# Kernel optimization log

Measured on AMD Instinct MI355X. Metric: run time of the kernel, lower is better.

## Reference

```python
import jax, jax.numpy as jnp
import numpy as np

N_NODES = 100000
N_EDGES = 1200000
NFEAT = 64
NHID = 64
NCLASS = 16
BN_EPS = 1e-5
L2_EPS = 1e-12


def setup_inputs() -> dict:
    key = jax.random.key(0)
    ks = jax.random.split(key, 8)
    edge_index = jax.random.randint(ks[0], (2, N_EDGES), 0, N_NODES, dtype=jnp.int64)
    x = jax.random.normal(ks[1], (N_NODES, NFEAT), dtype=jnp.float32)
    # SAGEConv params: lin_l (neighbor path, has bias), lin_r (root path, no bias)
    W_l = jax.random.normal(ks[2], (NHID, NFEAT), dtype=jnp.float32) * (1.0 / np.sqrt(NFEAT))
    b_l = jnp.zeros((NHID,), dtype=jnp.float32)
    W_r = jax.random.normal(ks[3], (NHID, NFEAT), dtype=jnp.float32) * (1.0 / np.sqrt(NFEAT))
    # BatchNorm1d affine params
    gamma = jnp.ones((NHID,), dtype=jnp.float32)
    beta = jnp.zeros((NHID,), dtype=jnp.float32)
    # final fc (xavier-ish scale, zero bias per weights_init)
    W_fc = jax.random.normal(ks[4], (NCLASS, NHID), dtype=jnp.float32) * (1.0 / np.sqrt(NHID))
    b_fc = jnp.zeros((NCLASS,), dtype=jnp.float32)
    return {"edge_index": edge_index, "x": x, "W_l": W_l, "b_l": b_l,
            "W_r": W_r, "gamma": gamma, "beta": beta, "W_fc": W_fc, "b_fc": b_fc}


def reference(edge_index, x, W_l, b_l, W_r, gamma, beta, W_fc, b_fc):
    N = x.shape[0]
    src, dst = edge_index[0], edge_index[1]
    # SAGEConv mean aggregation: gather x at source nodes, scatter-mean to dst
    msgs = x[src]                                                  # [E, F]
    sums = jax.ops.segment_sum(msgs, dst, num_segments=N)         # [N, F]
    cnt = jax.ops.segment_sum(jnp.ones((src.shape[0], 1), x.dtype), dst, num_segments=N)
    mean = sums / jnp.maximum(cnt, 1.0)
    # out = lin_l(mean_neighbors) + lin_r(x_root)
    h = mean @ W_l.T + b_l + x @ W_r.T                              # [N, H]
    # normalize=True -> L2 normalize rows (F.normalize semantics)
    h = h / jnp.maximum(jnp.linalg.norm(h, axis=-1, keepdims=True), L2_EPS)
    # transition: ReLU -> BatchNorm1d (training stats) -> Dropout (identity in eval)
    h = jax.nn.relu(h)
    mu = jnp.mean(h, axis=0)
    var = jnp.var(h, axis=0)
    h = (h - mu) / jnp.sqrt(var + BN_EPS) * gamma + beta
    return h @ W_fc.T + b_fc                                        # [N, C]
```

## Files before the change

kernel.cpp:

```cpp
#include <hip/hip_runtime.h>
#include <hip/hip_bf16.h>


typedef __attribute__((ext_vector_type(8))) short short8;
typedef __attribute__((ext_vector_type(4))) float f32x4;

__device__ __forceinline__ unsigned short f2bf(float f) {
    unsigned int u = __builtin_bit_cast(unsigned int, f);
    u += 0x7FFFu + ((u >> 16) & 1u);
    return (unsigned short)(u >> 16);
}
__device__ __forceinline__ float bf2f(unsigned short s) {
    return __builtin_bit_cast(float, ((unsigned int)s) << 16);
}

#define CHUNK 8192

__device__ __forceinline__ int exclScan256(int v, int* swv) {
    const int t = threadIdx.x, lane = t & 63, wid = t >> 6;
    __syncthreads();
    int s = v;
#pragma unroll
    for (int off = 1; off < 64; off <<= 1) {
        int tt = __shfl_up(s, off);
        if (lane >= off) s += tt;
    }
    if (lane == 63) swv[wid] = s;
    __syncthreads();
    if (t == 0) {
        int a = 0;
#pragma unroll
        for (int w = 0; w < 4; ++w) { int tt = swv[w]; swv[w] = a; a += tt; }
    }
    __syncthreads();
    return s - v + swv[wid];
}

__global__ __launch_bounds__(256) void k_prep(const int* __restrict__ eidx,
                                              int* __restrict__ cnt,
                                              const float4* __restrict__ x4,
                                              ushort4* __restrict__ xbf,
                                              int E, int NB, int NBLK,
                                              int n4, int do_x) {
    __shared__ int lh[256];
    const int tid = threadIdx.x;
    if ((int)blockIdx.x < NBLK) {
        lh[tid] = 0;
        __syncthreads();
        const int base = blockIdx.x * CHUNK;
        for (int i = tid; i < CHUNK; i += 256) {
            int e = base + i;
            if (e < E) atomicAdd(&lh[eidx[E + e] >> 9], 1);
        }
        __syncthreads();
        if (tid < NB) cnt[(size_t)tid * NBLK + blockIdx.x] = lh[tid];
    } else if (do_x) {
        int t = ((int)blockIdx.x - NBLK) * 256 + tid;
        if (t < n4) {
            float4 v = x4[t];
            xbf[t] = make_ushort4(f2bf(v.x), f2bf(v.y), f2bf(v.z), f2bf(v.w));
        }
    }
}

__global__ __launch_bounds__(256) void k_scanbkt(int* __restrict__ cnt,
                                                 int* __restrict__ btot,
                                                 int NBLK) {
    __shared__ int swv[4];
    const int b = blockIdx.x;
    const int t = threadIdx.x;
    int v = (t < NBLK) ? cnt[(size_t)b * NBLK + t] : 0;
    int excl = exclScan256(v, swv);
    if (t < NBLK) cnt[(size_t)b * NBLK + t] = excl;
    if (t == 255) btot[b] = excl + v;
}

__global__ __launch_bounds__(256) void k_bscatter(const int* __restrict__ eidx,
                                                  const int* __restrict__ cnt,
                                                  const int* __restrict__ btot,
                                                  unsigned int* __restrict__ ebuf,
                                                  int E, int NB, int NBLK) {
    __shared__ int cur[256];
    __shared__ int swv[4];
    const int tid = threadIdx.x;
    int bv = (tid < NB) ? btot[tid] : 0;
    int bexcl = exclScan256(bv, swv);
    if (tid < NB)
        cur[tid] = bexcl + cnt[(size_t)tid * NBLK + blockIdx.x];
    __syncthreads();
    const int base = blockIdx.x * CHUNK;
    for (int i = tid; i < CHUNK; i += 256) {
        int e = base + i;
        if (e < E) {
            int d = eidx[E + e];
            int s = eidx[e];
            int p = atomicAdd(&cur[d >> 9], 1);
            ebuf[p] = (unsigned int)s | ((unsigned int)(d & 511) << 17);
        }
    }
}

__global__ __launch_bounds__(256) void k_bfinal(const unsigned int* __restrict__ ebuf,
                                                const int* __restrict__ btot,
                                                int* __restrict__ rowptr,
                                                int* __restrict__ colv,
                                                int N, int NB, int E) {
    __shared__ int h[512];
    __shared__ int swv[4];
    __shared__ int sseg[2];
    const int b = blockIdx.x;
    const int tid = threadIdx.x;
    int bv = (tid < NB) ? btot[tid] : 0;
    int bexcl = exclScan256(bv, swv);
    if (tid == b) { sseg[0] = bexcl; sseg[1] = bexcl + bv; }
    h[2 * tid] = 0;
    h[2 * tid + 1] = 0;
    __syncthreads();
    const int segb = sseg[0], sege = sseg[1];
    for (int i = segb + tid; i < sege; i += 256)
        atomicAdd(&h[ebuf[i] >> 17], 1);
    __syncthreads();
    int a0 = h[2 * tid], a1 = h[2 * tid + 1];
    int ts = a0 + a1;
    const int lane = tid & 63, wid = tid >> 6;
    int s = ts;
#pragma unroll
    for (int off = 1; off < 64; off <<= 1) {
        int tt = __shfl_up(s, off);
        if (lane >= off) s += tt;
    }
    if (lane == 63) swv[wid] = s;
    __syncthreads();
    if (tid == 0) {
        int a = 0;
#pragma unroll
        for (int w = 0; w < 4; ++w) { int tt = swv[w]; swv[w] = a; a += tt; }
    }
    __syncthreads();
    int excl = s - ts + swv[wid];
    h[2 * tid] = excl;
    h[2 * tid + 1] = excl + a0;
    int node = b * 512 + 2 * tid;
    if (node < N) rowptr[node] = segb + excl;
    if (node + 1 < N) rowptr[node + 1] = segb + excl + a0;
    __syncthreads();
    for (int i = segb + tid; i < sege; i += 256) {
        unsigned int u = ebuf[i];
        int p = atomicAdd(&h[u >> 17], 1);
        colv[segb + p] = (int)(u & 0x1FFFFu);
    }
    if (b == 0 && tid == 0) rowptr[N] = E;
}

__device__ __forceinline__ void acc8(float a[8], uint4 v) {
    a[0] += bf2f((unsigned short)(v.x & 0xFFFFu));
    a[1] += bf2f((unsigned short)(v.x >> 16));
    a[2] += bf2f((unsigned short)(v.y & 0xFFFFu));
    a[3] += bf2f((unsigned short)(v.y >> 16));
    a[4] += bf2f((unsigned short)(v.z & 0xFFFFu));
    a[5] += bf2f((unsigned short)(v.z >> 16));
    a[6] += bf2f((unsigned short)(v.w & 0xFFFFu));
    a[7] += bf2f((unsigned short)(v.w >> 16));
}

__global__ __launch_bounds__(256) void k_gfused(
        const unsigned short* __restrict__ xbf,
        const int* __restrict__ rowptr, const int* __restrict__ colv,
        const float* __restrict__ Wl, const float* __restrict__ bl,
        const float* __restrict__ Wr,
        unsigned short* __restrict__ mh,
        float* __restrict__ pstats, int N) {
    __shared__ float sRed[4][128];

    const int tid = threadIdx.x;
    const int wid = tid >> 6;
    const int lane = tid & 63;
    const int l15 = lane & 15;
    const int quad = lane >> 4;

    const int tbase = blockIdx.x * 64 + wid * 16;
    const int mrow = tbase + l15;
    const int mld = (mrow < N) ? mrow : (N - 1);

    const int gb = rowptr[mld], ge = rowptr[mld + 1];
    float g0[8], g1[8];
#pragma unroll
    for (int j = 0; j < 8; ++j) { g0[j] = 0.f; g1[j] = 0.f; }
    const unsigned short* xrow = xbf + quad * 8;
    int p = gb;
    for (; p + 2 <= ge; p += 2) {
        int s0 = colv[p], s1 = colv[p + 1];
        uint4 v00 = *(const uint4*)(xrow + (size_t)s0 * 64);
        uint4 v01 = *(const uint4*)(xrow + (size_t)s0 * 64 + 32);
        uint4 v10 = *(const uint4*)(xrow + (size_t)s1 * 64);
        uint4 v11 = *(const uint4*)(xrow + (size_t)s1 * 64 + 32);
        acc8(g0, v00); acc8(g1, v01);
        acc8(g0, v10); acc8(g1, v11);
    }
    for (; p < ge; ++p) {
        int s0 = colv[p];
        uint4 v00 = *(const uint4*)(xrow + (size_t)s0 * 64);
        uint4 v01 = *(const uint4*)(xrow + (size_t)s0 * 64 + 32);
        acc8(g0, v00); acc8(g1, v01);
    }
    const float inv = 1.0f / fmaxf((float)(ge - gb), 1.0f);
    short8 afr[2];
    {
        union { short8 v; unsigned short u[8]; } pk;
#pragma unroll
        for (int j = 0; j < 8; ++j) pk.u[j] = f2bf(g0[j] * inv);
        afr[0] = pk.v;
#pragma unroll
        for (int j = 0; j < 8; ++j) pk.u[j] = f2bf(g1[j] * inv);
        afr[1] = pk.v;
    }

    short8 rfr[2];
    rfr[0] = *(const short8*)(xbf + (size_t)mld * 64 + quad * 8);
    rfr[1] = *(const short8*)(xbf + (size_t)mld * 64 + 32 + quad * 8);

    short8 bfrag[4][4];
#pragma unroll
    for (int c = 0; c < 4; ++c) {
#pragma unroll
        for (int f = 0; f < 4; ++f) {
            const int n = f * 16 + l15;
            const float* wsrc = (c < 2)
                ? (Wl + (size_t)n * 64 + c * 32 + quad * 8)
                : (Wr + (size_t)n * 64 + (c - 2) * 32 + quad * 8);
            float4 w0 = *(const float4*)wsrc;
            float4 w1 = *(const float4*)(wsrc + 4);
            union { short8 v; unsigned short u[8]; } pk;
            pk.u[0] = f2bf(w0.x); pk.u[1] = f2bf(w0.y);
            pk.u[2] = f2bf(w0.z); pk.u[3] = f2bf(w0.w);
            pk.u[4] = f2bf(w1.x); pk.u[5] = f2bf(w1.y);
            pk.u[6] = f2bf(w1.z); pk.u[7] = f2bf(w1.w);
            bfrag[c][f] = pk.v;
        }
    }
    float blv[4];
#pragma unroll
    for (int f = 0; f < 4; ++f) blv[f] = bl[f * 16 + l15];

    f32x4 acc[4] = {{0.f, 0.f, 0.f, 0.f}, {0.f, 0.f, 0.f, 0.f},
                    {0.f, 0.f, 0.f, 0.f}, {0.f, 0.f, 0.f, 0.f}};
#pragma unroll
    for (int c = 0; c < 2; ++c)
#pragma unroll
        for (int f = 0; f < 4; ++f)
            acc[f] = __builtin_amdgcn_mfma_f32_16x16x32_bf16(afr[c], bfrag[c][f], acc[f], 0, 0, 0);
#pragma unroll
    for (int c = 0; c < 2; ++c)
#pragma unroll
        for (int f = 0; f < 4; ++f)
            acc[f] = __builtin_amdgcn_mfma_f32_16x16x32_bf16(rfr[c], bfrag[c + 2][f], acc[f], 0, 0, 0);

    float psum[4] = {0.f, 0.f, 0.f, 0.f};
    float psq[4] = {0.f, 0.f, 0.f, 0.f};
#pragma unroll
    for (int reg = 0; reg < 4; ++reg) {
        const int node = tbase + quad * 4 + reg;
        float hv[4];
        float ss = 0.f;
#pragma unroll
        for (int f = 0; f < 4; ++f) {
            hv[f] = acc[f][reg] + blv[f];
            ss += hv[f] * hv[f];
        }
        ss += __shfl_xor(ss, 1);
        ss += __shfl_xor(ss, 2);
        ss += __shfl_xor(ss, 4);
        ss += __shfl_xor(ss, 8);
        float sc = 1.0f / fmaxf(sqrtf(ss), 1e-12f);
        if (node < N) {
#pragma unroll
            for (int f = 0; f < 4; ++f) {
                float r = fmaxf(hv[f] * sc, 0.f);
                unsigned short rb = f2bf(r);
                float e = bf2f(rb);
                mh[(size_t)node * 64 + f * 16 + l15] = rb;
                psum[f] += e;
                psq[f] += e * e;
            }
        }
    }

#pragma unroll
    for (int f = 0; f < 4; ++f) {
        psum[f] += __shfl_xor(psum[f], 16);
        psum[f] += __shfl_xor(psum[f], 32);
        psq[f] += __shfl_xor(psq[f], 16);
        psq[f] += __shfl_xor(psq[f], 32);
    }
    if (lane < 16) {
#pragma unroll
        for (int f = 0; f < 4; ++f) {
            sRed[wid][f * 16 + l15] = psum[f];
            sRed[wid][64 + f * 16 + l15] = psq[f];
        }
    }
    __syncthreads();
    if (tid < 128) {
        float v = sRed[0][tid] + sRed[1][tid] + sRed[2][tid] + sRed[3][tid];
        pstats[(size_t)blockIdx.x * 128 + tid] = v;
    }
}

__global__ __launch_bounds__(256) void k_gather_f32(
        const float4* __restrict__ x4, const int* __restrict__ rowptr,
        const int* __restrict__ colv, ushort4* __restrict__ mh, int N) {
    int t = blockIdx.x * 256 + threadIdx.x;
    int n = t >> 4;
    int l = t & 15;
    if (n >= N) return;
    int b = rowptr[n], e = rowptr[n + 1];
    float ax = 0.f, ay = 0.f, az = 0.f, aw = 0.f;
    int p = b;
    for (; p + 4 <= e; p += 4) {
        int s0 = colv[p], s1 = colv[p + 1], s2 = colv[p + 2], s3 = colv[p + 3];
        float4 v0 = x4[(size_t)s0 * 16 + l];
        float4 v1 = x4[(size_t)s1 * 16 + l];
        float4 v2 = x4[(size_t)s2 * 16 + l];
        float4 v3 = x4[(size_t)s3 * 16 + l];
        ax += (v0.x + v1.x) + (v2.x + v3.x);
        ay += (v0.y + v1.y) + (v2.y + v3.y);
        az += (v0.z + v1.z) + (v2.z + v3.z);
        aw += (v0.w + v1.w) + (v2.w + v3.w);
    }
    for (; p < e; ++p) {
        int s0 = colv[p];
        float4 v0 = x4[(size_t)s0 * 16 + l];
        ax += v0.x; ay += v0.y; az += v0.z; aw += v0.w;
    }
    float inv = 1.0f / fmaxf((float)(e - b), 1.0f);
    mh[(size_t)n * 16 + l] = make_ushort4(f2bf(ax * inv), f2bf(ay * inv),
                                          f2bf(az * inv), f2bf(aw * inv));
}

__global__ __launch_bounds__(256) void k_fused_legacy(
        const float* __restrict__ x,
        const float* __restrict__ Wl, const float* __restrict__ bl,
        const float* __restrict__ Wr,
        unsigned short* __restrict__ mh,
        float* __restrict__ pstats, int N) {
    __shared__ float sRed[4][128];
    const int tid = threadIdx.x;
    const int wid = tid >> 6;
    const int lane = tid & 63;
    const int l15 = lane & 15;
    const int quad = lane >> 4;

    short8 bfrag[4][4];
#pragma unroll
    for (int c = 0; c < 4; ++c) {
#pragma unroll
        for (int f = 0; f < 4; ++f) {
            const int n = f * 16 + l15;
            const float* wsrc = (c < 2)
                ? (Wl + (size_t)n * 64 + c * 32 + quad * 8)
                : (Wr + (size_t)n * 64 + (c - 2) * 32 + quad * 8);
            float4 w0 = *(const float4*)wsrc;
            float4 w1 = *(const float4*)(wsrc + 4);
            union { short8 v; unsigned short u[8]; } pk;
            pk.u[0] = f2bf(w0.x); pk.u[1] = f2bf(w0.y);
            pk.u[2] = f2bf(w0.z); pk.u[3] = f2bf(w0.w);
            pk.u[4] = f2bf(w1.x); pk.u[5] = f2bf(w1.y);
            pk.u[6] = f2bf(w1.z); pk.u[7] = f2bf(w1.w);
            bfrag[c][f] = pk.v;
        }
    }
    float blv[4];
#pragma unroll
    for (int f = 0; f < 4; ++f) blv[f] = bl[f * 16 + l15];

    const int tbase = blockIdx.x * 64 + wid * 16;
    const int mrow = tbase + l15;
    const int mld = (mrow < N) ? mrow : (N - 1);
    f32x4 acc[4] = {{0.f, 0.f, 0.f, 0.f}, {0.f, 0.f, 0.f, 0.f},
                    {0.f, 0.f, 0.f, 0.f}, {0.f, 0.f, 0.f, 0.f}};
#pragma unroll
    for (int c = 0; c < 2; ++c) {
        short8 a = *(const short8*)(mh + (size_t)mld * 64 + c * 32 + quad * 8);
#pragma unroll
        for (int f = 0; f < 4; ++f)
            acc[f] = __builtin_amdgcn_mfma_f32_16x16x32_bf16(a, bfrag[c][f], acc[f], 0, 0, 0);
    }
#pragma unroll
    for (int c = 0; c < 2; ++c) {
        const float* xp = x + (size_t)mld * 64 + c * 32 + quad * 8;
        float4 a0 = *(const float4*)xp;
        float4 a1 = *(const float4*)(xp + 4);
        union { short8 v; unsigned short u[8]; } pk;
        pk.u[0] = f2bf(a0.x); pk.u[1] = f2bf(a0.y);
        pk.u[2] = f2bf(a0.z); pk.u[3] = f2bf(a0.w);
        pk.u[4] = f2bf(a1.x); pk.u[5] = f2bf(a1.y);
        pk.u[6] = f2bf(a1.z); pk.u[7] = f2bf(a1.w);
#pragma unroll
        for (int f = 0; f < 4; ++f)
            acc[f] = __builtin_amdgcn_mfma_f32_16x16x32_bf16(pk.v, bfrag[c + 2][f], acc[f], 0, 0, 0);
    }

    float psum[4] = {0.f, 0.f, 0.f, 0.f};
    float psq[4] = {0.f, 0.f, 0.f, 0.f};
#pragma unroll
    for (int reg = 0; reg < 4; ++reg) {
        const int node = tbase + quad * 4 + reg;
        float hv[4];
        float ss = 0.f;
#pragma unroll
        for (int f = 0; f < 4; ++f) {
            hv[f] = acc[f][reg] + blv[f];
            ss += hv[f] * hv[f];
        }
        ss += __shfl_xor(ss, 1);
        ss += __shfl_xor(ss, 2);
        ss += __shfl_xor(ss, 4);
        ss += __shfl_xor(ss, 8);
        float sc = 1.0f / fmaxf(sqrtf(ss), 1e-12f);
        if (node < N) {
#pragma unroll
            for (int f = 0; f < 4; ++f) {
                float r = fmaxf(hv[f] * sc, 0.f);
                unsigned short rb = f2bf(r);
                float e = bf2f(rb);
                mh[(size_t)node * 64 + f * 16 + l15] = rb;
                psum[f] += e;
                psq[f] += e * e;
            }
        }
    }
#pragma unroll
    for (int f = 0; f < 4; ++f) {
        psum[f] += __shfl_xor(psum[f], 16);
        psum[f] += __shfl_xor(psum[f], 32);
        psq[f] += __shfl_xor(psq[f], 16);
        psq[f] += __shfl_xor(psq[f], 32);
    }
    if (lane < 16) {
#pragma unroll
        for (int f = 0; f < 4; ++f) {
            sRed[wid][f * 16 + l15] = psum[f];
            sRed[wid][64 + f * 16 + l15] = psq[f];
        }
    }
    __syncthreads();
    if (tid < 128) {
        float v = sRed[0][tid] + sRed[1][tid] + sRed[2][tid] + sRed[3][tid];
        pstats[(size_t)blockIdx.x * 128 + tid] = v;
    }
}

__global__ __launch_bounds__(64) void k_stats(const float* __restrict__ pstats,
                                              float* __restrict__ stats, int nblk) {
    int col = blockIdx.x;
    int l = threadIdx.x;
    float s = 0.f;
    for (int r = l; r < nblk; r += 64) s += pstats[(size_t)r * 128 + col];
    s += __shfl_xor(s, 1);
    s += __shfl_xor(s, 2);
    s += __shfl_xor(s, 4);
    s += __shfl_xor(s, 8);
    s += __shfl_xor(s, 16);
    s += __shfl_xor(s, 32);
    if (l == 0) stats[col] = s;
}

__global__ __launch_bounds__(256) void k_out(
        const unsigned short* __restrict__ h, const float* __restrict__ stats,
        const float* __restrict__ gamma, const float* __restrict__ beta,
        const float* __restrict__ Wfc, const float* __restrict__ bfc,
        float* __restrict__ out, int N) {
    __shared__ float sWm[64 * 16];
    __shared__ float sShift[64];
    __shared__ float sBase[16];
    const int tid = threadIdx.x;
    const float invN = 1.0f / (float)N;
    if (tid < 64) {
        float mu = stats[tid] * invN;
        float var = stats[64 + tid] * invN - mu * mu;
        float sc = gamma[tid] / sqrtf(var + 1e-5f);
        sShift[tid] = beta[tid] - mu * sc;
#pragma unroll
        for (int c = 0; c < 16; ++c) sWm[tid * 16 + c] = Wfc[c * 64 + tid] * sc;
    }
    __syncthreads();
    if (tid < 16) {
        float b = bfc[tid];
#pragma unroll
        for (int j = 0; j < 64; ++j) b += sShift[j] * Wfc[tid * 64 + j];
        sBase[tid] = b;
    }
    __syncthreads();
    int g = blockIdx.x * 256 + tid;
    int n = g >> 4;
    int c = g & 15;
    if (n >= N) return;
    const ushort4* h4 = (const ushort4*)(h + (size_t)n * 64);
    float acc = sBase[c];
#pragma unroll
    for (int jq = 0; jq < 16; ++jq) {
        ushort4 v = h4[jq];
        acc += bf2f(v.x) * sWm[(jq * 4 + 0) * 16 + c];
        acc += bf2f(v.y) * sWm[(jq * 4 + 1) * 16 + c];
        acc += bf2f(v.z) * sWm[(jq * 4 + 2) * 16 + c];
        acc += bf2f(v.w) * sWm[(jq * 4 + 3) * 16 + c];
    }
    out[(size_t)n * 16 + c] = acc;
}

extern "C" void kernel_launch(void* const* d_in, const int* in_sizes, int n_in,
                              void* d_out, int out_size, void* d_ws, size_t ws_size,
                              hipStream_t stream) {
    const int* eidx = (const int*)d_in[0];
    const float* x = (const float*)d_in[1];
    const float* Wl = (const float*)d_in[2];
    const float* bl = (const float*)d_in[3];
    const float* Wr = (const float*)d_in[4];
    const float* gamma = (const float*)d_in[5];
    const float* beta = (const float*)d_in[6];
    const float* Wfc = (const float*)d_in[7];
    const float* bfc = (const float*)d_in[8];
    float* out = (float*)d_out;

    const int E = in_sizes[0] / 2;
    const int N = in_sizes[1] / 64;
    const int NB = (N + 511) >> 9;
    const int NBLK = (E + CHUNK - 1) / CHUNK;
    const int fb = (N + 63) / 64;
    const int n4 = N * 16;

    int* cnt = (int*)d_ws;
    int* btot = cnt + (size_t)NB * NBLK;
    int* rowptr = btot + NB;
    float* pstats = (float*)(rowptr + N + 1);
    float* stats = pstats + (size_t)fb * 128;
    int* colv = (int*)(stats + 128);
    unsigned int* ebuf = (unsigned int*)(colv + E);
    unsigned short* mh = (unsigned short*)(((uintptr_t)(ebuf + E) + 15) & ~(uintptr_t)15);
    unsigned short* xbf = mh + (size_t)N * 64;

    size_t need_bf = (size_t)((char*)(xbf + (size_t)N * 64) - (char*)d_ws);
    const int use_bf = (ws_size >= need_bf) ? 1 : 0;

    int cbl = use_bf ? (n4 + 255) / 256 : 0;
    k_prep<<<NBLK + cbl, 256, 0, stream>>>(eidx, cnt, (const float4*)x,
                                           (ushort4*)xbf, E, NB, NBLK, n4, use_bf);
    k_scanbkt<<<NB, 256, 0, stream>>>(cnt, btot, NBLK);
    k_bscatter<<<NBLK, 256, 0, stream>>>(eidx, cnt, btot, ebuf, E, NB, NBLK);
    k_bfinal<<<NB, 256, 0, stream>>>(ebuf, btot, rowptr, colv, N, NB, E);

    if (use_bf) {
        k_gfused<<<fb, 256, 0, stream>>>(xbf, rowptr, colv, Wl, bl, Wr,
                                         mh, pstats, N);
    } else {
        int gblocks = (int)(((size_t)N * 16 + 255) / 256);
        k_gather_f32<<<gblocks, 256, 0, stream>>>((const float4*)x, rowptr, colv,
                                                  (ushort4*)mh, N);
        k_fused_legacy<<<fb, 256, 0, stream>>>(x, Wl, bl, Wr, mh, pstats, N);
    }

    k_stats<<<128, 64, 0, stream>>>(pstats, stats, fb);

    int oblocks = (int)(((size_t)N * 16 + 255) / 256);
    k_out<<<oblocks, 256, 0, stream>>>(mh, stats, gamma, beta, Wfc, bfc, out, N);
}
```

Before: 231.0 us.

## Spread neighbor gather across 16 lanes per node and stage means in LDS

The fused gather+GEMM kernel now processes 16 nodes per block. All 256 threads gather neighbor rows, with 16 lanes per node each loading 8 bytes, instead of one lane per node loading 128 bytes. The bf16 means go through shared memory, and a single wave then runs the MFMA projection with the weight fragments converted inline. This raises memory-level parallelism in the irregular gather, but leaves three of four waves idle during the MFMA and normalization phase. It also multiplies the number of blocks, weight loads and partial-stat rows that k_stats must reduce.

```diff
diff --git a/kernel.cpp b/kernel.cpp
--- a/kernel.cpp
+++ b/kernel.cpp
@@ -152,17 +152,6 @@
     if (b == 0 && tid == 0) rowptr[N] = E;
 }
 
-__device__ __forceinline__ void acc8(float a[8], uint4 v) {
-    a[0] += bf2f((unsigned short)(v.x & 0xFFFFu));
-    a[1] += bf2f((unsigned short)(v.x >> 16));
-    a[2] += bf2f((unsigned short)(v.y & 0xFFFFu));
-    a[3] += bf2f((unsigned short)(v.y >> 16));
-    a[4] += bf2f((unsigned short)(v.z & 0xFFFFu));
-    a[5] += bf2f((unsigned short)(v.z >> 16));
-    a[6] += bf2f((unsigned short)(v.w & 0xFFFFu));
-    a[7] += bf2f((unsigned short)(v.w >> 16));
-}
-
 __global__ __launch_bounds__(256) void k_gfused(
         const unsigned short* __restrict__ xbf,
         const int* __restrict__ rowptr, const int* __restrict__ colv,
@@ -170,56 +159,68 @@
         const float* __restrict__ Wr,
         unsigned short* __restrict__ mh,
         float* __restrict__ pstats, int N) {
-    __shared__ float sRed[4][128];
+    __shared__ unsigned short sm[16][72];
 
     const int tid = threadIdx.x;
-    const int wid = tid >> 6;
-    const int lane = tid & 63;
+    const int tbase = blockIdx.x * 16;
+
+    {
+        const int nloc = tid >> 4;
+        const int l = tid & 15;
+        const int mrow = tbase + nloc;
+        const int mld = (mrow < N) ? mrow : (N - 1);
+        const uint2* xbf2 = (const uint2*)xbf;
+        int b = rowptr[mld], e = rowptr[mld + 1];
+        float a0 = 0.f, a1 = 0.f, a2 = 0.f, a3 = 0.f;
+        int p = b;
+        for (; p + 4 <= e; p += 4) {
+            int s0 = colv[p], s1 = colv[p + 1], s2 = colv[p + 2], s3 = colv[p + 3];
+            uint2 v0 = xbf2[(size_t)s0 * 16 + l];
+            uint2 v1 = xbf2[(size_t)s1 * 16 + l];
+            uint2 v2 = xbf2[(size_t)s2 * 16 + l];
+            uint2 v3 = xbf2[(size_t)s3 * 16 + l];
+            a0 += bf2f((unsigned short)(v0.x & 0xFFFF)) + bf2f((unsigned short)(v1.x & 0xFFFF)) +
+                  bf2f((unsigned short)(v2.x & 0xFFFF)) + bf2f((unsigned short)(v3.x & 0xFFFF));
+            a1 += bf2f((unsigned short)(v0.x >> 16)) + bf2f((unsigned short)(v1.x >> 16)) +
+                  bf2f((unsigned short)(v2.x >> 16)) + bf2f((unsigned short)(v3.x >> 16));
+            a2 += bf2f((unsigned short)(v0.y & 0xFFFF)) + bf2f((unsigned short)(v1.y & 0xFFFF)) +
+                  bf2f((unsigned short)(v2.y & 0xFFFF)) + bf2f((unsigned short)(v3.y & 0xFFFF));
+            a3 += bf2f((unsigned short)(v0.y >> 16)) + bf2f((unsigned short)(v1.y >> 16)) +
+                  bf2f((unsigned short)(v2.y >> 16)) + bf2f((unsigned short)(v3.y >> 16));
+        }
+        for (; p < e; ++p) {
+            int s0 = colv[p];
+            uint2 v0 = xbf2[(size_t)s0 * 16 + l];
+            a0 += bf2f((unsigned short)(v0.x & 0xFFFF));
+            a1 += bf2f((unsigned short)(v0.x >> 16));
+            a2 += bf2f((unsigned short)(v0.y & 0xFFFF));
+            a3 += bf2f((unsigned short)(v0.y >> 16));
+        }
+        float inv = 1.0f / fmaxf((float)(e - b), 1.0f);
+        *(ushort4*)&sm[nloc][l * 4] = make_ushort4(f2bf(a0 * inv), f2bf(a1 * inv),
+                                                   f2bf(a2 * inv), f2bf(a3 * inv));
+    }
+    __syncthreads();
+    if (tid >= 64) return;
+
+    const int lane = tid;
     const int l15 = lane & 15;
     const int quad = lane >> 4;
 
-    const int tbase = blockIdx.x * 64 + wid * 16;
-    const int mrow = tbase + l15;
-    const int mld = (mrow < N) ? mrow : (N - 1);
-
-    const int gb = rowptr[mld], ge = rowptr[mld + 1];
-    float g0[8], g1[8];
-#pragma unroll
-    for (int j = 0; j < 8; ++j) { g0[j] = 0.f; g1[j] = 0.f; }
-    const unsigned short* xrow = xbf + quad * 8;
-    int p = gb;
-    for (; p + 2 <= ge; p += 2) {
-        int s0 = colv[p], s1 = colv[p + 1];
-        uint4 v00 = *(const uint4*)(xrow + (size_t)s0 * 64);
-        uint4 v01 = *(const uint4*)(xrow + (size_t)s0 * 64 + 32);
-        uint4 v10 = *(const uint4*)(xrow + (size_t)s1 * 64);
-        uint4 v11 = *(const uint4*)(xrow + (size_t)s1 * 64 + 32);
-        acc8(g0, v00); acc8(g1, v01);
-        acc8(g0, v10); acc8(g1, v11);
-    }
-    for (; p < ge; ++p) {
-        int s0 = colv[p];
-        uint4 v00 = *(const uint4*)(xrow + (size_t)s0 * 64);
-        uint4 v01 = *(const uint4*)(xrow + (size_t)s0 * 64 + 32);
-        acc8(g0, v00); acc8(g1, v01);
-    }
-    const float inv = 1.0f / fmaxf((float)(ge - gb), 1.0f);
-    short8 afr[2];
-    {
-        union { short8 v; unsigned short u[8]; } pk;
-#pragma unroll
-        for (int j = 0; j < 8; ++j) pk.u[j] = f2bf(g0[j] * inv);
-        afr[0] = pk.v;
-#pragma unroll
-        for (int j = 0; j < 8; ++j) pk.u[j] = f2bf(g1[j] * inv);
-        afr[1] = pk.v;
-    }
-
-    short8 rfr[2];
-    rfr[0] = *(const short8*)(xbf + (size_t)mld * 64 + quad * 8);
-    rfr[1] = *(const short8*)(xbf + (size_t)mld * 64 + 32 + quad * 8);
-
-    short8 bfrag[4][4];
+    short8 afr[2], rfr[2];
+    afr[0] = *(const short8*)&sm[l15][quad * 8];
+    afr[1] = *(const short8*)&sm[l15][32 + quad * 8];
+    const int rrow = tbase + l15;
+    const int rld = (rrow < N) ? rrow : (N - 1);
+    rfr[0] = *(const short8*)(xbf + (size_t)rld * 64 + quad * 8);
+    rfr[1] = *(const short8*)(xbf + (size_t)rld * 64 + 32 + quad * 8);
+
+    float blv[4];
+#pragma unroll
+    for (int f = 0; f < 4; ++f) blv[f] = bl[f * 16 + l15];
+
+    f32x4 acc[4] = {{0.f, 0.f, 0.f, 0.f}, {0.f, 0.f, 0.f, 0.f},
+                    {0.f, 0.f, 0.f, 0.f}, {0.f, 0.f, 0.f, 0.f}};
 #pragma unroll
     for (int c = 0; c < 4; ++c) {
 #pragma unroll
@@ -235,25 +236,10 @@
             pk.u[2] = f2bf(w0.z); pk.u[3] = f2bf(w0.w);
             pk.u[4] = f2bf(w1.x); pk.u[5] = f2bf(w1.y);
             pk.u[6] = f2bf(w1.z); pk.u[7] = f2bf(w1.w);
-            bfrag[c][f] = pk.v;
-        }
-    }
-    float blv[4];
-#pragma unroll
-    for (int f = 0; f < 4; ++f) blv[f] = bl[f * 16 + l15];
-
-    f32x4 acc[4] = {{0.f, 0.f, 0.f, 0.f}, {0.f, 0.f, 0.f, 0.f},
-                    {0.f, 0.f, 0.f, 0.f}, {0.f, 0.f, 0.f, 0.f}};
-#pragma unroll
-    for (int c = 0; c < 2; ++c)
-#pragma unroll
-        for (int f = 0; f < 4; ++f)
-            acc[f] = __builtin_amdgcn_mfma_f32_16x16x32_bf16(afr[c], bfrag[c][f], acc[f], 0, 0, 0);
-#pragma unroll
-    for (int c = 0; c < 2; ++c)
-#pragma unroll
-        for (int f = 0; f < 4; ++f)
-            acc[f] = __builtin_amdgcn_mfma_f32_16x16x32_bf16(rfr[c], bfrag[c + 2][f], acc[f], 0, 0, 0);
+            acc[f] = __builtin_amdgcn_mfma_f32_16x16x32_bf16(
+                (c < 2) ? afr[c] : rfr[c - 2], pk.v, acc[f], 0, 0, 0);
+        }
+    }
 
     float psum[4] = {0.f, 0.f, 0.f, 0.f};
     float psq[4] = {0.f, 0.f, 0.f, 0.f};
@@ -295,14 +281,9 @@
     if (lane < 16) {
 #pragma unroll
         for (int f = 0; f < 4; ++f) {
-            sRed[wid][f * 16 + l15] = psum[f];
-            sRed[wid][64 + f * 16 + l15] = psq[f];
-        }
-    }
-    __syncthreads();
-    if (tid < 128) {
-        float v = sRed[0][tid] + sRed[1][tid] + sRed[2][tid] + sRed[3][tid];
-        pstats[(size_t)blockIdx.x * 128 + tid] = v;
+            pstats[(size_t)blockIdx.x * 128 + f * 16 + l15] = psum[f];
+            pstats[(size_t)blockIdx.x * 128 + 64 + f * 16 + l15] = psq[f];
+        }
     }
 }
 
@@ -526,14 +507,15 @@
     const int N = in_sizes[1] / 64;
     const int NB = (N + 511) >> 9;
     const int NBLK = (E + CHUNK - 1) / CHUNK;
-    const int fb = (N + 63) / 64;
+    const int fbG = (N + 15) / 16;
+    const int fbL = (N + 63) / 64;
     const int n4 = N * 16;
 
     int* cnt = (int*)d_ws;
     int* btot = cnt + (size_t)NB * NBLK;
     int* rowptr = btot + NB;
     float* pstats = (float*)(rowptr + N + 1);
-    float* stats = pstats + (size_t)fb * 128;
+    float* stats = pstats + (size_t)fbG * 128;
     int* colv = (int*)(stats + 128);
     unsigned int* ebuf = (unsigned int*)(colv + E);
     unsigned short* mh = (unsigned short*)(((uintptr_t)(ebuf + E) + 15) & ~(uintptr_t)15);
@@ -550,16 +532,16 @@
     k_bfinal<<<NB, 256, 0, stream>>>(ebuf, btot, rowptr, colv, N, NB, E);
 
     if (use_bf) {
-        k_gfused<<<fb, 256, 0, stream>>>(xbf, rowptr, colv, Wl, bl, Wr,
-                                         mh, pstats, N);
+        k_gfused<<<fbG, 256, 0, stream>>>(xbf, rowptr, colv, Wl, bl, Wr,
+                                          mh, pstats, N);
+        k_stats<<<128, 64, 0, stream>>>(pstats, stats, fbG);
     } else {
         int gblocks = (int)(((size_t)N * 16 + 255) / 256);
         k_gather_f32<<<gblocks, 256, 0, stream>>>((const float4*)x, rowptr, colv,
                                                   (ushort4*)mh, N);
-        k_fused_legacy<<<fb, 256, 0, stream>>>(x, Wl, bl, Wr, mh, pstats, N);
-    }
-
-    k_stats<<<128, 64, 0, stream>>>(pstats, stats, fb);
+        k_fused_legacy<<<fbL, 256, 0, stream>>>(x, Wl, bl, Wr, mh, pstats, N);
+        k_stats<<<128, 64, 0, stream>>>(pstats, stats, fbL);
+    }
 
     int oblocks = (int)(((size_t)N * 16 + 255) / 256);
     k_out<<<oblocks, 256, 0, stream>>>(mh, stats, gamma, beta, Wfc, bfc, out, N);
```

Result: slower. 245.3 us (+6.2%).
